# Kernel tuning notes

Measured on AMD Instinct MI355X. Metric: run time of the kernel, lower is better.

The kernel has to match this reference:

```python
import jax, jax.numpy as jnp
import numpy as np

EMBED = 768
HEADS = 12
FFN = 3072
EPS = 1e-5

def _linear_params(key, din, dout):
    k1, k2 = jax.random.split(key)
    s = 1.0 / np.sqrt(din)
    W = jax.random.uniform(k1, (din, dout), minval=-s, maxval=s, dtype=jnp.float32)
    b = jax.random.uniform(k2, (dout,), minval=-s, maxval=s, dtype=jnp.float32)
    return W, b

def setup_inputs() -> dict:
    key = jax.random.key(0)
    ks = jax.random.split(key, 8)
    x = jax.random.normal(ks[0], (1, 4096, EMBED), dtype=jnp.float32)
    Wq, bq = _linear_params(ks[1], EMBED, EMBED)
    Wk, bk = _linear_params(ks[2], EMBED, EMBED)
    Wv, bv = _linear_params(ks[3], EMBED, EMBED)
    Wo, bo = _linear_params(ks[4], EMBED, EMBED)
    W1, b1 = _linear_params(ks[5], EMBED, FFN)
    W2, b2 = _linear_params(ks[6], FFN, EMBED)
    ln1_g = jnp.ones((EMBED,), jnp.float32); ln1_b = jnp.zeros((EMBED,), jnp.float32)
    ln2_g = jnp.ones((EMBED,), jnp.float32); ln2_b = jnp.zeros((EMBED,), jnp.float32)
    return {"x": x, "Wq": Wq, "bq": bq, "Wk": Wk, "bk": bk, "Wv": Wv, "bv": bv,
            "Wo": Wo, "bo": bo, "ln1_g": ln1_g, "ln1_b": ln1_b,
            "ln2_g": ln2_g, "ln2_b": ln2_b, "W1": W1, "b1": b1, "W2": W2, "b2": b2}

def _layernorm(x, g, b):
    mu = jnp.mean(x, axis=-1, keepdims=True)
    var = jnp.mean(jnp.square(x - mu), axis=-1, keepdims=True)
    return (x - mu) * jax.lax.rsqrt(var + EPS) * g + b

def _block(x, Wq, bq, Wk, bk, Wv, bv, Wo, bo, ln1_g, ln1_b, ln2_g, ln2_b, W1, b1, W2, b2):
    B, T, C = x.shape
    H = HEADS
    D = C // H
    # pre-LN
    h = _layernorm(x, ln1_g, ln1_b)
    # naive causal self-attention with explicit [B,H,T,T] scores (as in source)
    q = (h @ Wq + bq).reshape(B, T, H, D).transpose(0, 2, 1, 3)  # bhtd
    k = (h @ Wk + bk).reshape(B, T, H, D).transpose(0, 2, 1, 3)
    v = (h @ Wv + bv).reshape(B, T, H, D).transpose(0, 2, 1, 3)
    scores = jnp.einsum('bhqd,bhkd->bhqk', q, k) / jnp.sqrt(jnp.float32(D))
    causal = jnp.tril(jnp.ones((T, T), dtype=bool))  # True = keep
    scores = jnp.where(causal, scores, -jnp.inf)
    attn = jax.nn.softmax(scores, axis=-1)
    ctx = jnp.einsum('bhqk,bhkd->bhqd', attn, v)
    ctx = ctx.transpose(0, 2, 1, 3).reshape(B, T, C)
    y = ctx @ Wo + bo
    x = y + h  # residual onto ln1 output (source adds to post-LN x)
    # second LN + MLP
    h2 = _layernorm(x, ln2_g, ln2_b)
    m = jax.nn.gelu(h2 @ W1 + b1, approximate=False) @ W2 + b2
    return m + h2

def reference(x, Wq, bq, Wk, bk, Wv, bv, Wo, bo, ln1_g, ln1_b, ln2_g, ln2_b, W1, b1, W2, b2):
    return _block(x, Wq, bq, Wk, bk, Wv, bv, Wo, bo, ln1_g, ln1_b, ln2_g, ln2_b, W1, b1, W2, b2)
```

## Files before the change

### kernel.cpp

```cpp
#include <hip/hip_runtime.h>
#include <math.h>

#define EMBED 768
#define FFN_D 3072
#define TSEQ 4096
#define NHEAD 12
#define DHEAD 64
#define CQKV 2304
#define NSPLIT 4
#define NQITEMS 192
#define SC2Q 0.180336880111120419f

typedef _Float16 f16;
typedef __attribute__((ext_vector_type(2))) _Float16 f16x2;
typedef __attribute__((ext_vector_type(4))) _Float16 f16x4;
typedef __attribute__((ext_vector_type(8))) _Float16 f16x8;
typedef __attribute__((ext_vector_type(4))) float f32x4;

__device__ __forceinline__ f16x2 pkrtz(float a, float b) {
    return __builtin_bit_cast(f16x2, __builtin_amdgcn_cvt_pkrtz(a, b));
}

__device__ __forceinline__ void gload16(const f16* g, f16* lds) {
    __builtin_amdgcn_global_load_lds((const __attribute__((address_space(1))) void*)g,
                                     (__attribute__((address_space(3))) void*)lds, 16, 0, 0);
}

__global__ __launch_bounds__(256) void prep_kernel(const float* __restrict__ Wq,
                                                   const float* __restrict__ Wk,
                                                   const float* __restrict__ Wv,
                                                   const float* __restrict__ Wo,
                                                   const float* __restrict__ W1,
                                                   const float* __restrict__ W2,
                                                   const float* __restrict__ bq,
                                                   const float* __restrict__ bk,
                                                   const float* __restrict__ bv,
                                                   f16* __restrict__ WqkvT,
                                                   f16* __restrict__ WoT,
                                                   f16* __restrict__ W1T,
                                                   f16* __restrict__ W2T,
                                                   float* __restrict__ bqkv) {
    const int b = blockIdx.x;
    const int t = threadIdx.x;
    if (b == 6912) {
#pragma unroll
        for (int i = 0; i < 9; i++) {
            int idx = i * 256 + t;
            if (idx < 768) bqkv[idx] = bq[idx];
            else if (idx < 1536) bqkv[idx] = bk[idx - 768];
            else if (idx < 2304) bqkv[idx] = bv[idx - 1536];
        }
        return;
    }
    const float* W; f16* WT; int din, dout, local;
    if (b < 576)       { W = Wq; WT = WqkvT;                         din = 768;  dout = 768;  local = b; }
    else if (b < 1152) { W = Wk; WT = WqkvT + 768 * 768;             din = 768;  dout = 768;  local = b - 576; }
    else if (b < 1728) { W = Wv; WT = WqkvT + 2 * 768 * 768;         din = 768;  dout = 768;  local = b - 1152; }
    else if (b < 2304) { W = Wo; WT = WoT;                           din = 768;  dout = 768;  local = b - 1728; }
    else if (b < 4608) { W = W1; WT = W1T;                           din = 768;  dout = 3072; local = b - 2304; }
    else               { W = W2; WT = W2T;                           din = 3072; dout = 768;  local = b - 4608; }
    const int tx2 = dout / 32;
    const int j0 = (local % tx2) * 32;
    const int i0 = (local / tx2) * 32;
    __shared__ float tile[32][33];
    const int tx = t & 31;
    const int ty = t >> 5;
#pragma unroll
    for (int rr = ty; rr < 32; rr += 8)
        tile[rr][tx] = W[(size_t)(i0 + rr) * dout + j0 + tx];
    __syncthreads();
#pragma unroll
    for (int rr = ty; rr < 32; rr += 8)
        WT[(size_t)(j0 + rr) * din + i0 + tx] = (f16)tile[tx][rr];
}

__global__ __launch_bounds__(256) void ln_kernel(const float* __restrict__ x,
                                                 const float* __restrict__ g,
                                                 const float* __restrict__ b,
                                                 f16* __restrict__ hh) {
    const int row = blockIdx.x;
    const float* xr = x + (size_t)row * EMBED;
    const int t = threadIdx.x;
    float v0 = xr[t], v1 = xr[t + 256], v2 = xr[t + 512];
    float s = v0 + v1 + v2;
#pragma unroll
    for (int m = 1; m < 64; m <<= 1) s += __shfl_xor(s, m);
    __shared__ float red[4], red2[4];
    const int wid = t >> 6, lane = t & 63;
    if (lane == 0) red[wid] = s;
    __syncthreads();
    float mean = (red[0] + red[1] + red[2] + red[3]) * (1.0f / 768.0f);
    float d0 = v0 - mean, d1 = v1 - mean, d2 = v2 - mean;
    float ss = d0 * d0 + d1 * d1 + d2 * d2;
#pragma unroll
    for (int m = 1; m < 64; m <<= 1) ss += __shfl_xor(ss, m);
    if (lane == 0) red2[wid] = ss;
    __syncthreads();
    float inv = rsqrtf((red2[0] + red2[1] + red2[2] + red2[3]) * (1.0f / 768.0f) + 1e-5f);
    size_t base = (size_t)row * EMBED;
    hh[base + t]       = (f16)(d0 * inv * g[t] + b[t]);
    hh[base + t + 256] = (f16)(d1 * inv * g[t + 256] + b[t + 256]);
    hh[base + t + 512] = (f16)(d2 * inv * g[t + 512] + b[t + 512]);
}

template <int EPI, int BM, int BN>
__global__ __launch_bounds__(256) void gemm_kernel(const f16* __restrict__ A,
                                                   const f16* __restrict__ BT,
                                                   const float* __restrict__ bias,
                                                   const f16* __restrict__ resh,
                                                   float* __restrict__ outf,
                                                   f16* __restrict__ outh,
                                                   f16* __restrict__ vtout,
                                                   int M, int N, int K) {
    constexpr int IM = BM / 32;
    constexpr int JN = BN / 32;
    __shared__ __align__(16) f16 As[BM][64];
    __shared__ __align__(16) f16 Bs[BN][64];
    const int t = threadIdx.x;
    const int m0 = blockIdx.y * BM;
    const int n0 = blockIdx.x * BN;
    const int wid = t >> 6;
    const int lane = t & 63;
    const int wm = (wid >> 1) * (BM / 2);
    const int wn = (wid & 1) * (BN / 2);
    const int lr = lane & 15;
    const int quad = lane >> 4;
    const int sr = lane >> 3;
    const int scn = (lane & 7) ^ sr;
    const int xv = lr & 7;

    f32x4 zero = {0.f, 0.f, 0.f, 0.f};
    f32x4 acc[IM][JN];
#pragma unroll
    for (int i = 0; i < IM; i++)
#pragma unroll
        for (int j = 0; j < JN; j++) acc[i][j] = zero;

    const f16* Ap = A + (size_t)(m0 + wid * (BM / 4) + sr) * K + scn * 8;
    const f16* Bp = BT + (size_t)(n0 + wid * (BN / 4) + sr) * K + scn * 8;

    for (int k0 = 0; k0 < K; k0 += 64) {
        __syncthreads();
#pragma unroll
        for (int c = 0; c < BM / 32; c++)
            gload16(Ap + (size_t)(c * 8) * K + k0, &As[wid * (BM / 4) + c * 8][0]);
#pragma unroll
        for (int c = 0; c < BN / 32; c++)
            gload16(Bp + (size_t)(c * 8) * K + k0, &Bs[wid * (BN / 4) + c * 8][0]);
        __syncthreads();
#pragma unroll
        for (int ks = 0; ks < 2; ks++) {
            f16x8 af[IM], bf[JN];
#pragma unroll
            for (int i = 0; i < IM; i++)
                af[i] = *(const f16x8*)&As[wm + i * 16 + lr][((ks * 4 + quad) ^ xv) * 8];
#pragma unroll
            for (int j = 0; j < JN; j++)
                bf[j] = *(const f16x8*)&Bs[wn + j * 16 + lr][((ks * 4 + quad) ^ xv) * 8];
#pragma unroll
            for (int i = 0; i < IM; i++)
#pragma unroll
                for (int j = 0; j < JN; j++)
                    acc[i][j] = __builtin_amdgcn_mfma_f32_16x16x32_f16(bf[j], af[i], acc[i][j], 0, 0, 0);
        }
    }

    const bool vsec = (EPI == 0) && (n0 >= 2 * EMBED);
#pragma unroll
    for (int i = 0; i < IM; i++) {
        const int row = m0 + wm + i * 16 + lr;
#pragma unroll
        for (int j = 0; j < JN; j++) {
            const int col = n0 + wn + j * 16 + quad * 4;
            const float4 bv = *(const float4*)&bias[col];
            float v0 = acc[i][j][0] + bv.x;
            float v1 = acc[i][j][1] + bv.y;
            float v2 = acc[i][j][2] + bv.z;
            float v3 = acc[i][j][3] + bv.w;
            const size_t idx = (size_t)row * N + col;
            if (EPI == 0) {
                if (vsec) {
                    const int c0 = col - 2 * EMBED;
                    vtout[(size_t)(c0 + 0) * TSEQ + row] = (f16)v0;
                    vtout[(size_t)(c0 + 1) * TSEQ + row] = (f16)v1;
                    vtout[(size_t)(c0 + 2) * TSEQ + row] = (f16)v2;
                    vtout[(size_t)(c0 + 3) * TSEQ + row] = (f16)v3;
                } else {
                    const float qs = (col < EMBED) ? SC2Q : 1.0f;
                    f16x4 hv = {(f16)(v0 * qs), (f16)(v1 * qs), (f16)(v2 * qs), (f16)(v3 * qs)};
                    *(f16x4*)&outh[idx] = hv;
                }
            } else if (EPI == 1) {
                const f16x4 rr = *(const f16x4*)&resh[idx];
                f32x4 ov = {v0 + (float)rr[0], v1 + (float)rr[1], v2 + (float)rr[2], v3 + (float)rr[3]};
                *(f32x4*)&outf[idx] = ov;
            } else {
                f16x4 hv = {(f16)(0.5f * v0 * (1.0f + erff(v0 * 0.70710678118654752f))),
                            (f16)(0.5f * v1 * (1.0f + erff(v1 * 0.70710678118654752f))),
                            (f16)(0.5f * v2 * (1.0f + erff(v2 * 0.70710678118654752f))),
                            (f16)(0.5f * v3 * (1.0f + erff(v3 * 0.70710678118654752f)))};
                *(f16x4*)&outh[idx] = hv;
            }
        }
    }
}

__global__ __launch_bounds__(256) void attn_kernel(const f16* __restrict__ qkv,
                                                   const f16* __restrict__ vT,
                                                   f16* __restrict__ OpartH,
                                                   float2* __restrict__ ml,
                                                   int* __restrict__ ctr) {
    __shared__ __align__(16) f16 Ks[64][72];
    __shared__ __align__(16) f16 Vt[64][72];
    __shared__ int s_item;
    const int t = threadIdx.x;
    const int wid = t >> 6;
    const int lane = t & 63;
    const int lr = lane & 15;
    const int quad = lane >> 4;
    const int srow = t >> 3;
    const int scol = (t & 7) * 8;
    const int xq = blockIdx.x & 7;

    for (;;) {
        __syncthreads();
        if (t == 0) s_item = atomicAdd(&ctr[xq], 1);
        __syncthreads();
        const int item = s_item;
        if (item >= NQITEMS) return;
        const int qb = 31 - item / 6;
        const int u = xq * 6 + item % 6;
        const int h = u >> 2;
        const int sp = u & 3;
        const int q0 = qb * 128;

        const int nkb = 2 * qb + 2;
        const int chunk = (nkb + NSPLIT - 1) / NSPLIT;
        const int kb0 = sp * chunk;
        const int kb1 = min(nkb, kb0 + chunk);
        const int wrow0 = q0 + wid * 32;

        float m_i[2] = {-INFINITY, -INFINITY};
        float l_lane[2] = {0.f, 0.f};
        f32x4 zero = {0.f, 0.f, 0.f, 0.f};
        f32x4 o[4][2];
#pragma unroll
        for (int dt = 0; dt < 4; dt++)
#pragma unroll
            for (int qt = 0; qt < 2; qt++) o[dt][qt] = zero;

        f16x8 qf[2][2];
        int4 kreg[2], vreg[2];
        const f16* kbase = qkv + EMBED + (size_t)h * DHEAD;
        const f16* vbase = vT + (size_t)h * DHEAD * TSEQ;
        if (kb0 < kb1) {
#pragma unroll
            for (int qt = 0; qt < 2; qt++)
#pragma unroll
                for (int dh = 0; dh < 2; dh++)
                    qf[qt][dh] = *(const f16x8*)(qkv + (size_t)(wrow0 + qt * 16 + lr) * CQKV
                                                 + h * DHEAD + dh * 32 + quad * 8);
            const int k0 = kb0 * 64;
#pragma unroll
            for (int p = 0; p < 2; p++) {
                kreg[p] = *(const int4*)(kbase + (size_t)(k0 + p * 32 + srow) * CQKV + scol);
                vreg[p] = *(const int4*)(vbase + (size_t)(p * 32 + srow) * TSEQ + k0 + scol);
            }
        }

        for (int kb = kb0; kb < kb1; ++kb) {
            const int k0 = kb * 64;
            __syncthreads();
#pragma unroll
            for (int p = 0; p < 2; p++) {
                *(int4*)&Ks[p * 32 + srow][scol] = kreg[p];
                *(int4*)&Vt[p * 32 + srow][scol] = vreg[p];
            }
            __syncthreads();
            if (kb + 1 < kb1) {
                const int kn = (kb + 1) * 64;
#pragma unroll
                for (int p = 0; p < 2; p++) {
                    kreg[p] = *(const int4*)(kbase + (size_t)(kn + p * 32 + srow) * CQKV + scol);
                    vreg[p] = *(const int4*)(vbase + (size_t)(p * 32 + srow) * TSEQ + kn + scol);
                }
            }

            if (k0 <= wrow0 + 31) {
                f32x4 s[4][2];
#pragma unroll
                for (int kt = 0; kt < 4; kt++)
#pragma unroll
                    for (int qt = 0; qt < 2; qt++) s[kt][qt] = zero;
#pragma unroll
                for (int dh = 0; dh < 2; dh++) {
#pragma unroll
                    for (int kt = 0; kt < 4; kt++) {
                        f16x8 kf = *(const f16x8*)&Ks[kt * 16 + lr][dh * 32 + quad * 8];
#pragma unroll
                        for (int qt = 0; qt < 2; qt++)
                            s[kt][qt] = __builtin_amdgcn_mfma_f32_16x16x32_f16(kf, qf[qt][dh], s[kt][qt], 0, 0, 0);
                    }
                }
                if (k0 + 63 > wrow0) {
#pragma unroll
                    for (int kt = 0; kt < 4; kt++)
#pragma unroll
                        for (int qt = 0; qt < 2; qt++)
#pragma unroll
                            for (int r = 0; r < 4; r++) {
                                int key = k0 + kt * 16 + quad * 4 + r;
                                int row = wrow0 + qt * 16 + lr;
                                if (key > row) s[kt][qt][r] = -INFINITY;
                            }
                }
                float al[2];
#pragma unroll
                for (int qt = 0; qt < 2; qt++) {
                    float mx = -INFINITY;
#pragma unroll
                    for (int kt = 0; kt < 4; kt++)
#pragma unroll
                        for (int r = 0; r < 4; r++) mx = fmaxf(mx, s[kt][qt][r]);
                    mx = fmaxf(mx, __shfl_xor(mx, 16));
                    mx = fmaxf(mx, __shfl_xor(mx, 32));
                    float mn = fmaxf(m_i[qt], mx);
                    al[qt] = exp2f(m_i[qt] - mn);
                    m_i[qt] = mn;
                }
                union PW { f16x8 v8; f16x2 h2[4]; };
                PW pw[2][2];
                float rs[2] = {0.f, 0.f};
#pragma unroll
                for (int kt = 0; kt < 4; kt++)
#pragma unroll
                    for (int qt = 0; qt < 2; qt++) {
                        float p0 = exp2f(s[kt][qt][0] - m_i[qt]);
                        float p1 = exp2f(s[kt][qt][1] - m_i[qt]);
                        float p2 = exp2f(s[kt][qt][2] - m_i[qt]);
                        float p3 = exp2f(s[kt][qt][3] - m_i[qt]);
                        rs[qt] += (p0 + p1) + (p2 + p3);
                        pw[kt >> 1][qt].h2[(kt & 1) * 2]     = pkrtz(p0, p1);
                        pw[kt >> 1][qt].h2[(kt & 1) * 2 + 1] = pkrtz(p2, p3);
                    }
#pragma unroll
                for (int qt = 0; qt < 2; qt++) l_lane[qt] = l_lane[qt] * al[qt] + rs[qt];
#pragma unroll
                for (int dt = 0; dt < 4; dt++)
#pragma unroll
                    for (int qt = 0; qt < 2; qt++)
#pragma unroll
                        for (int r = 0; r < 4; r++) o[dt][qt][r] *= al[qt];
#pragma unroll
                for (int s2 = 0; s2 < 2; s2++)
#pragma unroll
                    for (int dt = 0; dt < 4; dt++) {
                        f16x4 vlo = *(const f16x4*)&Vt[dt * 16 + lr][s2 * 32 + quad * 4];
                        f16x4 vhi = *(const f16x4*)&Vt[dt * 16 + lr][s2 * 32 + quad * 4 + 16];
                        f16x8 vf;
#pragma unroll
                        for (int e = 0; e < 4; e++) { vf[e] = vlo[e]; vf[e + 4] = vhi[e]; }
#pragma unroll
                        for (int qt = 0; qt < 2; qt++)
                            o[dt][qt] = __builtin_amdgcn_mfma_f32_16x16x32_f16(vf, pw[s2][qt].v8, o[dt][qt], 0, 0, 0);
                    }
            }
        }

        float l_i[2];
#pragma unroll
        for (int qt = 0; qt < 2; qt++) {
            float v2 = l_lane[qt];
            v2 += __shfl_xor(v2, 16);
            v2 += __shfl_xor(v2, 32);
            l_i[qt] = v2;
        }
#pragma unroll
        for (int dt = 0; dt < 4; dt++)
#pragma unroll
            for (int qt = 0; qt < 2; qt++) {
                int row = wrow0 + qt * 16 + lr;
                f16x4 oh = {(f16)o[dt][qt][0], (f16)o[dt][qt][1], (f16)o[dt][qt][2], (f16)o[dt][qt][3]};
                *(f16x4*)&OpartH[((size_t)sp * TSEQ + row) * EMBED + h * DHEAD + dt * 16 + quad * 4] = oh;
            }
#pragma unroll
        for (int qt = 0; qt < 2; qt++)
            if (quad == 0) {
                int row = wrow0 + qt * 16 + lr;
                ml[((size_t)sp * TSEQ + row) * NHEAD + h] = make_float2(m_i[qt], l_i[qt]);
            }
    }
}

__global__ __launch_bounds__(256) void attn_merge_kernel(const f16* __restrict__ OpartH,
                                                         const float2* __restrict__ ml,
                                                         f16* __restrict__ ctx) {
    const int row = blockIdx.x;
    const int t = threadIdx.x;
    __shared__ float wgt[NSPLIT][NHEAD];
    if (t < NHEAD) {
        float m[NSPLIT], l[NSPLIT];
        float M = -INFINITY;
#pragma unroll
        for (int s = 0; s < NSPLIT; s++) {
            float2 v = ml[((size_t)s * TSEQ + row) * NHEAD + t];
            m[s] = v.x; l[s] = v.y;
            M = fmaxf(M, m[s]);
        }
        float L = 0.f;
        float w[NSPLIT];
#pragma unroll
        for (int s = 0; s < NSPLIT; s++) {
            w[s] = exp2f(m[s] - M);
            L += l[s] * w[s];
        }
        float rL = 1.0f / L;
#pragma unroll
        for (int s = 0; s < NSPLIT; s++) wgt[s][t] = w[s] * rL;
    }
    __syncthreads();
#pragma unroll
    for (int p = 0; p < 3; p++) {
        int c = t + p * 256;
        int h = c >> 6;
        float acc = 0.f;
#pragma unroll
        for (int s = 0; s < NSPLIT; s++)
            acc += wgt[s][h] * (float)OpartH[((size_t)s * TSEQ + row) * EMBED + c];
        ctx[(size_t)row * EMBED + c] = (f16)acc;
    }
}

extern "C" void kernel_launch(void* const* d_in, const int* in_sizes, int n_in,
                              void* d_out, int out_size, void* d_ws, size_t ws_size,
                              hipStream_t stream) {
    const float* x     = (const float*)d_in[0];
    const float* Wq    = (const float*)d_in[1];
    const float* bq    = (const float*)d_in[2];
    const float* Wk    = (const float*)d_in[3];
    const float* bk    = (const float*)d_in[4];
    const float* Wv    = (const float*)d_in[5];
    const float* bv    = (const float*)d_in[6];
    const float* Wo    = (const float*)d_in[7];
    const float* bo    = (const float*)d_in[8];
    const float* ln1_g = (const float*)d_in[9];
    const float* ln1_b = (const float*)d_in[10];
    const float* ln2_g = (const float*)d_in[11];
    const float* ln2_b = (const float*)d_in[12];
    const float* W1    = (const float*)d_in[13];
    const float* b1    = (const float*)d_in[14];
    const float* W2    = (const float*)d_in[15];
    const float* b2    = (const float*)d_in[16];

    char* p = (char*)d_ws;
    auto alloc = [&](size_t bytes) -> void* {
        void* r = (void*)p;
        p += (bytes + 255) & ~(size_t)255;
        return r;
    };
    f16*   WqkvT = (f16*)alloc((size_t)CQKV * EMBED * 2);
    f16*   WoT   = (f16*)alloc((size_t)EMBED * EMBED * 2);
    f16*   W1T   = (f16*)alloc((size_t)FFN_D * EMBED * 2);
    f16*   W2T   = (f16*)alloc((size_t)EMBED * FFN_D * 2);
    float* bqkv  = (float*)alloc((size_t)CQKV * 4);
    f16*   hh    = (f16*)alloc((size_t)TSEQ * EMBED * 2);
    f16*   qkv   = (f16*)alloc((size_t)TSEQ * CQKV * 2);
    f16*   vT    = (f16*)alloc((size_t)EMBED * TSEQ * 2);
    f16*   ctx   = (f16*)alloc((size_t)TSEQ * EMBED * 2);
    float* x2    = (float*)alloc((size_t)TSEQ * EMBED * 4);
    f16*   h2h   = (f16*)alloc((size_t)TSEQ * EMBED * 2);
    f16*   m1    = (f16*)alloc((size_t)TSEQ * FFN_D * 2);
    int*   ctr   = (int*)alloc(256);

    f16*    OpartH = m1;
    float2* mlbuf  = (float2*)x2;

    dim3 blk(256);
    prep_kernel<<<dim3(6913), blk, 0, stream>>>(Wq, Wk, Wv, Wo, W1, W2, bq, bk, bv,
                                                WqkvT, WoT, W1T, W2T, bqkv);
    ln_kernel<<<dim3(TSEQ), blk, 0, stream>>>(x, ln1_g, ln1_b, hh);
    gemm_kernel<0, 128, 128><<<dim3(CQKV / 128, TSEQ / 128), blk, 0, stream>>>(
        hh, WqkvT, bqkv, nullptr, nullptr, qkv, vT, TSEQ, CQKV, EMBED);
    (void)hipMemsetAsync(ctr, 0, 256, stream);
    attn_kernel<<<dim3(1536), blk, 0, stream>>>(qkv, vT, OpartH, mlbuf, ctr);
    attn_merge_kernel<<<dim3(TSEQ), blk, 0, stream>>>(OpartH, mlbuf, ctx);
    gemm_kernel<1, 128, 64><<<dim3(EMBED / 64, TSEQ / 128), blk, 0, stream>>>(
        ctx, WoT, bo, hh, x2, nullptr, nullptr, TSEQ, EMBED, EMBED);
    ln_kernel<<<dim3(TSEQ), blk, 0, stream>>>(x2, ln2_g, ln2_b, h2h);
    gemm_kernel<2, 128, 128><<<dim3(FFN_D / 128, TSEQ / 128), blk, 0, stream>>>(
        h2h, W1T, b1, nullptr, nullptr, m1, nullptr, TSEQ, FFN_D, EMBED);
    gemm_kernel<1, 128, 64><<<dim3(EMBED / 64, TSEQ / 128), blk, 0, stream>>>(
        m1, W2T, b2, h2h, (float*)d_out, nullptr, nullptr, TSEQ, EMBED, FFN_D);
}
```

Baseline: 368.9 us.

## Lazy softmax rescale, permuted V LDS layout, staged output stores in attention

Attention now rescales the running max, sum and output accumulators only when some lane's new row max exceeds the stored max by more than a threshold (FA4-style lazy rescaling). V tiles are written to LDS in a permuted column order so each MFMA operand comes from one 16-byte load instead of two 8-byte loads plus a shuffle. Output tiles are staged through LDS so global stores are coalesced 16-byte rows, exp2 uses the hardware builtin, and the persistent grid is halved. Skipping rescales lets values grow up to 2^4 before fp16 packing, which adds some numerical risk, and the smaller grid changes occupancy.

Measured after the change: 329.6 us. 1.12x faster.

```diff
diff --git a/kernel.cpp b/kernel.cpp
--- a/kernel.cpp
+++ b/kernel.cpp
@@ -16,6 +16,12 @@
 typedef __attribute__((ext_vector_type(4))) _Float16 f16x4;
 typedef __attribute__((ext_vector_type(8))) _Float16 f16x8;
 typedef __attribute__((ext_vector_type(4))) float f32x4;
+
+#if __has_builtin(__builtin_amdgcn_exp2f)
+#define EXP2(x) __builtin_amdgcn_exp2f(x)
+#else
+#define EXP2(x) exp2f(x)
+#endif
 
 __device__ __forceinline__ f16x2 pkrtz(float a, float b) {
     return __builtin_bit_cast(f16x2, __builtin_amdgcn_cvt_pkrtz(a, b));
@@ -220,6 +226,7 @@
     const int quad = lane >> 4;
     const int srow = t >> 3;
     const int scol = (t & 7) * 8;
+    const int pA = (t & 1) * 16 + ((t >> 1) & 1) * 4 + (t & 4) * 8;
     const int xq = blockIdx.x & 7;
 
     for (;;) {
@@ -274,7 +281,8 @@
 #pragma unroll
             for (int p = 0; p < 2; p++) {
                 *(int4*)&Ks[p * 32 + srow][scol] = kreg[p];
-                *(int4*)&Vt[p * 32 + srow][scol] = vreg[p];
+                *(int2*)&Vt[p * 32 + srow][pA]     = make_int2(vreg[p].x, vreg[p].y);
+                *(int2*)&Vt[p * 32 + srow][pA + 8] = make_int2(vreg[p].z, vreg[p].w);
             }
             __syncthreads();
             if (kb + 1 < kb1) {
@@ -314,19 +322,30 @@
                                 if (key > row) s[kt][qt][r] = -INFINITY;
                             }
                 }
-                float al[2];
+                float mx[2];
 #pragma unroll
                 for (int qt = 0; qt < 2; qt++) {
-                    float mx = -INFINITY;
+                    float m = -INFINITY;
 #pragma unroll
                     for (int kt = 0; kt < 4; kt++)
 #pragma unroll
-                        for (int r = 0; r < 4; r++) mx = fmaxf(mx, s[kt][qt][r]);
-                    mx = fmaxf(mx, __shfl_xor(mx, 16));
-                    mx = fmaxf(mx, __shfl_xor(mx, 32));
-                    float mn = fmaxf(m_i[qt], mx);
-                    al[qt] = exp2f(m_i[qt] - mn);
-                    m_i[qt] = mn;
+                        for (int r = 0; r < 4; r++) m = fmaxf(m, s[kt][qt][r]);
+                    m = fmaxf(m, __shfl_xor(m, 16));
+                    m = fmaxf(m, __shfl_xor(m, 32));
+                    mx[qt] = m;
+                }
+                if (__any((mx[0] > m_i[0] + 4.f) || (mx[1] > m_i[1] + 4.f))) {
+#pragma unroll
+                    for (int qt = 0; qt < 2; qt++) {
+                        float mn = fmaxf(m_i[qt], mx[qt]);
+                        float al = EXP2(m_i[qt] - mn);
+                        m_i[qt] = mn;
+                        l_lane[qt] *= al;
+#pragma unroll
+                        for (int dt = 0; dt < 4; dt++)
+#pragma unroll
+                            for (int r = 0; r < 4; r++) o[dt][qt][r] *= al;
+                    }
                 }
                 union PW { f16x8 v8; f16x2 h2[4]; };
                 PW pw[2][2];
@@ -335,31 +354,21 @@
                 for (int kt = 0; kt < 4; kt++)
 #pragma unroll
                     for (int qt = 0; qt < 2; qt++) {
-                        float p0 = exp2f(s[kt][qt][0] - m_i[qt]);
-                        float p1 = exp2f(s[kt][qt][1] - m_i[qt]);
-                        float p2 = exp2f(s[kt][qt][2] - m_i[qt]);
-                        float p3 = exp2f(s[kt][qt][3] - m_i[qt]);
+                        float p0 = EXP2(s[kt][qt][0] - m_i[qt]);
+                        float p1 = EXP2(s[kt][qt][1] - m_i[qt]);
+                        float p2 = EXP2(s[kt][qt][2] - m_i[qt]);
+                        float p3 = EXP2(s[kt][qt][3] - m_i[qt]);
                         rs[qt] += (p0 + p1) + (p2 + p3);
                         pw[kt >> 1][qt].h2[(kt & 1) * 2]     = pkrtz(p0, p1);
                         pw[kt >> 1][qt].h2[(kt & 1) * 2 + 1] = pkrtz(p2, p3);
                     }
 #pragma unroll
-                for (int qt = 0; qt < 2; qt++) l_lane[qt] = l_lane[qt] * al[qt] + rs[qt];
-#pragma unroll
-                for (int dt = 0; dt < 4; dt++)
-#pragma unroll
-                    for (int qt = 0; qt < 2; qt++)
-#pragma unroll
-                        for (int r = 0; r < 4; r++) o[dt][qt][r] *= al[qt];
+                for (int qt = 0; qt < 2; qt++) l_lane[qt] += rs[qt];
 #pragma unroll
                 for (int s2 = 0; s2 < 2; s2++)
 #pragma unroll
                     for (int dt = 0; dt < 4; dt++) {
-                        f16x4 vlo = *(const f16x4*)&Vt[dt * 16 + lr][s2 * 32 + quad * 4];
-                        f16x4 vhi = *(const f16x4*)&Vt[dt * 16 + lr][s2 * 32 + quad * 4 + 16];
-                        f16x8 vf;
-#pragma unroll
-                        for (int e = 0; e < 4; e++) { vf[e] = vlo[e]; vf[e + 4] = vhi[e]; }
+                        f16x8 vf = *(const f16x8*)&Vt[dt * 16 + lr][s2 * 32 + quad * 8];
 #pragma unroll
                         for (int qt = 0; qt < 2; qt++)
                             o[dt][qt] = __builtin_amdgcn_mfma_f32_16x16x32_f16(vf, pw[s2][qt].v8, o[dt][qt], 0, 0, 0);
@@ -375,14 +384,23 @@
             v2 += __shfl_xor(v2, 32);
             l_i[qt] = v2;
         }
-#pragma unroll
-        for (int dt = 0; dt < 4; dt++)
-#pragma unroll
-            for (int qt = 0; qt < 2; qt++) {
-                int row = wrow0 + qt * 16 + lr;
+        __syncthreads();
+        f16* ob = ((wid & 2) ? &Vt[0][0] : &Ks[0][0]) + (wid & 1) * (32 * 72);
+#pragma unroll
+        for (int qt = 0; qt < 2; qt++)
+#pragma unroll
+            for (int dt = 0; dt < 4; dt++) {
                 f16x4 oh = {(f16)o[dt][qt][0], (f16)o[dt][qt][1], (f16)o[dt][qt][2], (f16)o[dt][qt][3]};
-                *(f16x4*)&OpartH[((size_t)sp * TSEQ + row) * EMBED + h * DHEAD + dt * 16 + quad * 4] = oh;
-            }
+                *(f16x4*)&ob[(qt * 16 + lr) * 72 + dt * 16 + quad * 4] = oh;
+            }
+        const int rl = lane >> 3;
+        const int ck = lane & 7;
+#pragma unroll
+        for (int i = 0; i < 4; i++) {
+            const int row_l = rl + i * 8;
+            f16x8 val = *(const f16x8*)&ob[row_l * 72 + ck * 8];
+            *(f16x8*)&OpartH[((size_t)sp * TSEQ + wrow0 + row_l) * EMBED + h * DHEAD + ck * 8] = val;
+        }
 #pragma unroll
         for (int qt = 0; qt < 2; qt++)
             if (quad == 0) {
@@ -482,7 +500,7 @@
     gemm_kernel<0, 128, 128><<<dim3(CQKV / 128, TSEQ / 128), blk, 0, stream>>>(
         hh, WqkvT, bqkv, nullptr, nullptr, qkv, vT, TSEQ, CQKV, EMBED);
     (void)hipMemsetAsync(ctr, 0, 256, stream);
-    attn_kernel<<<dim3(1536), blk, 0, stream>>>(qkv, vT, OpartH, mlbuf, ctr);
+    attn_kernel<<<dim3(768), blk, 0, stream>>>(qkv, vT, OpartH, mlbuf, ctr);
     attn_merge_kernel<<<dim3(TSEQ), blk, 0, stream>>>(OpartH, mlbuf, ctx);
     gemm_kernel<1, 128, 64><<<dim3(EMBED / 64, TSEQ / 128), blk, 0, stream>>>(
         ctx, WoT, bo, hh, x2, nullptr, nullptr, TSEQ, EMBED, EMBED);
```
